# Kernel optimization log

Hardware: AMD Instinct MI355X
Metric: run time of the kernel (lower is better)

Reference implementation:

```python
import jax, jax.numpy as jnp
import numpy as np

EPS = 1e-12

def _l2norm(v, axis):
    n = jnp.sqrt(jnp.sum(v * v, axis=axis, keepdims=True))
    return v / jnp.maximum(n, EPS)

def setup_inputs() -> dict:
    key = jax.random.key(0)
    k1, k2, k3, k4 = jax.random.split(key, 4)
    N, T, D, K = 8, 2048, 512, 64
    x = jax.random.normal(k1, (N, T, D), dtype=jnp.float32)
    W = jax.random.normal(k2, (K, D), dtype=jnp.float32) * (1.0 / np.sqrt(D))  # Conv1d(k=1) weight squeezed
    b = jax.random.normal(k3, (K,), dtype=jnp.float32) * 0.01
    centroids = jax.random.uniform(k4, (K, D), dtype=jnp.float32)
    return {"x": x, "W": W, "b": b, "centroids": centroids}

def reference(x, W, b, centroids):
    N, T, D = x.shape
    K = centroids.shape[0]
    # L2-normalize descriptors along feature dim
    xn = _l2norm(x, axis=2)                                  # [N,T,D]
    # Conv1d with kernel_size=1 == per-timestep linear: [N,K,T] logits over clusters
    logits = jnp.einsum('ntd,kd->nkt', xn, W) + b[None, :, None]
    a = jax.nn.softmax(logits, axis=1)                       # soft assignment over K
    # Algebraically equal to sum_t a[n,k,t] * (xn[n,t,:] - c[k,:])
    vlad = jnp.einsum('nkt,ntd->nkd', a, xn) \
         - jnp.sum(a, axis=2)[:, :, None] * centroids[None]  # [N,K,D]
    vlad = _l2norm(vlad, axis=2)                             # intra-normalize per cluster
    vlad = vlad.reshape(N, K * D)
    return _l2norm(vlad, axis=1)                             # global L2 normalize
```

## Files before the change

### kernel.cpp

```cpp
#include <hip/hip_runtime.h>
#include <math.h>

#define EPS 1e-12f
#define NN 8
#define TT 2048
#define DD 512
#define KK 64

typedef short short8 __attribute__((ext_vector_type(8)));
typedef float floatx4 __attribute__((ext_vector_type(4)));

__device__ __forceinline__ unsigned short f2bf(float f) {
    unsigned int u = __float_as_uint(f);
    u += 0x7FFFu + ((u >> 16) & 1u);
    return (unsigned short)(u >> 16);
}
__device__ __forceinline__ unsigned int pack2(float a, float b) {
    return (unsigned int)f2bf(a) | ((unsigned int)f2bf(b) << 16);
}


__global__ __launch_bounds__(256) void kA(const float* __restrict__ x,
                                          const float* __restrict__ W,
                                          const float* __restrict__ bias,
                                          unsigned short* __restrict__ xb,
                                          unsigned short* __restrict__ aTs,
                                          float* __restrict__ asumP) {
    __shared__ unsigned short sW[32768];
    __shared__ float sRed[256];

    const int tid = threadIdx.x;

    const int w = tid >> 6, lane = tid & 63;
    const int l = lane & 15, q = lane >> 4;
    const int row0 = blockIdx.x * 64 + w * 16;
    const int row = row0 + l;
    const int n = row0 >> 11;
    const int tl0 = row0 & (TT - 1);

    const float* xr = x + (size_t)row * DD;
    unsigned short* xo = xb + (size_t)row * DD;
    short8 fragA[16];
    float ssq = 0.0f;
#pragma unroll
    for (int s = 0; s < 16; ++s) {
        float4 u0 = *(const float4*)(xr + s * 32 + q * 8);
        float4 u1 = *(const float4*)(xr + s * 32 + q * 8 + 4);
        ssq += u0.x*u0.x + u0.y*u0.y + u0.z*u0.z + u0.w*u0.w
             + u1.x*u1.x + u1.y*u1.y + u1.z*u1.z + u1.w*u1.w;
        uint4 pk;
        pk.x = pack2(u0.x, u0.y); pk.y = pack2(u0.z, u0.w);
        pk.z = pack2(u1.x, u1.y); pk.w = pack2(u1.z, u1.w);
        union { uint4 u; short8 s8; } cvt; cvt.u = pk;
        fragA[s] = cvt.s8;
        *(uint4*)(xo + s * 32 + q * 8) = pk;
    }

    {
        const int sp = tid >> 4, hp = (tid >> 2) & 3, qp = tid & 3;
        const float* wsrc = W + (size_t)(hp * 16) * DD + sp * 32 + qp * 8;
        unsigned short* wdst = sW + (size_t)tid * 128;
#pragma unroll
        for (int j = 0; j < 16; ++j) {
            float4 u0 = *(const float4*)(wsrc + (size_t)j * DD);
            float4 u1 = *(const float4*)(wsrc + (size_t)j * DD + 4);
            uint4 pk;
            pk.x = pack2(u0.x, u0.y); pk.y = pack2(u0.z, u0.w);
            pk.z = pack2(u1.x, u1.y); pk.w = pack2(u1.z, u1.w);
            *(uint4*)(wdst + j * 8) = pk;
        }
    }

    ssq += __shfl_xor(ssq, 16, 64);
    ssq += __shfl_xor(ssq, 32, 64);
    float st = 1.0f / fmaxf(sqrtf(ssq), EPS);

    __syncthreads();

    floatx4 acc[4];
#pragma unroll
    for (int h = 0; h < 4; ++h) acc[h] = floatx4{0.f, 0.f, 0.f, 0.f};
#pragma unroll
    for (int s = 0; s < 16; ++s) {
#pragma unroll
        for (int h = 0; h < 4; ++h) {
            short8 wf = *(const short8*)(sW + ((size_t)((s * 4 + h) * 64) + lane) * 8);
            acc[h] = __builtin_amdgcn_mfma_f32_16x16x32_bf16(fragA[s], wf, acc[h], 0, 0, 0);
        }
    }

    float sr[4];
#pragma unroll
    for (int r = 0; r < 4; ++r) sr[r] = __shfl(st, 4 * q + r, 64);
    float bj[4];
#pragma unroll
    for (int h = 0; h < 4; ++h) bj[h] = bias[h * 16 + l];

    float av[4][4];
#pragma unroll
    for (int r = 0; r < 4; ++r) {
        float v0 = acc[0][r] * sr[r] + bj[0], v1 = acc[1][r] * sr[r] + bj[1];
        float v2 = acc[2][r] * sr[r] + bj[2], v3 = acc[3][r] * sr[r] + bj[3];
        float m = fmaxf(fmaxf(v0, v1), fmaxf(v2, v3));
#pragma unroll
        for (int msk = 1; msk <= 8; msk <<= 1) m = fmaxf(m, __shfl_xor(m, msk, 64));
        float e0 = __expf(v0 - m), e1 = __expf(v1 - m), e2 = __expf(v2 - m), e3 = __expf(v3 - m);
        float ss = e0 + e1 + e2 + e3;
#pragma unroll
        for (int msk = 1; msk <= 8; msk <<= 1) ss += __shfl_xor(ss, msk, 64);
        float inv = 1.0f / ss;
        av[0][r] = e0 * inv; av[1][r] = e1 * inv; av[2][r] = e2 * inv; av[3][r] = e3 * inv;
    }

#pragma unroll
    for (int h = 0; h < 4; ++h) {
        uint2 p;
        p.x = pack2(av[h][0] * sr[0], av[h][1] * sr[1]);
        p.y = pack2(av[h][2] * sr[2], av[h][3] * sr[3]);
        *(uint2*)(aTs + ((size_t)(n * KK + h * 16 + l)) * TT + tl0 + 4 * q) = p;
    }

#pragma unroll
    for (int h = 0; h < 4; ++h) {
        float sh = av[h][0] + av[h][1] + av[h][2] + av[h][3];
        sh += __shfl_xor(sh, 16, 64);
        sh += __shfl_xor(sh, 32, 64);
        if (q == 0) sRed[w * 64 + h * 16 + l] = sh;
    }
    __syncthreads();
    if (tid < 64) {
        float s0 = sRed[tid] + sRed[64 + tid] + sRed[128 + tid] + sRed[192 + tid];
        asumP[(size_t)blockIdx.x * 64 + tid] = s0;
    }
}

__global__ __launch_bounds__(256) void kB(const unsigned short* __restrict__ xb,
                                          const unsigned short* __restrict__ aTs,
                                          float* __restrict__ part) {
    __shared__ unsigned char smem[17408];
    unsigned short* sX0 = (unsigned short*)smem;
    unsigned short* sX1 = sX0 + 4096;
    float* sT = (float*)smem;

    const int tid = threadIdx.x;
    const int wv = tid >> 6, lane = tid & 63;
    const int l = lane & 15, q = lane >> 4;
    const int bid = blockIdx.x;
    const int low = bid & 63;
    const int n = low >> 3, tc = low & 7, dt = bid >> 6;

    const int ts = tid & 63, dq = tid >> 6;
    const unsigned short* xbase = xb + ((size_t)(n * TT + tc * 256)) * DD + dt * 64 + dq * 16;
    const int g = ts >> 3, t7 = ts & 7;

#define STAGE(S, BUF)                                                          \
    {                                                                          \
        const unsigned short* p_ = xbase + (size_t)((S) * 64 + ts) * DD;       \
        unsigned short vals[16];                                               \
        *(uint4*)(vals) = *(const uint4*)(p_);                                 \
        *(uint4*)(vals + 8) = *(const uint4*)(p_ + 8);                         \
        _Pragma("unroll")                                                      \
        for (int e = 0; e < 16; ++e) {                                         \
            int d_ = dq * 16 + e;                                              \
            (BUF)[d_ * 64 + ((g ^ (d_ & 7)) << 3) + t7] = vals[e];             \
        }                                                                      \
    }

    floatx4 acc[4];
#pragma unroll
    for (int nt = 0; nt < 4; ++nt) acc[nt] = floatx4{0.f, 0.f, 0.f, 0.f};
    const unsigned short* abase = aTs + ((size_t)(n * KK + wv * 16 + l)) * TT + tc * 256;

    STAGE(0, sX0);
    __syncthreads();
#pragma unroll
    for (int s = 0; s < 4; ++s) {
        unsigned short* cur = (s & 1) ? sX1 : sX0;
        unsigned short* nxt = (s & 1) ? sX0 : sX1;
        if (s < 3) {
            if (s == 0) STAGE(1, nxt)
            else if (s == 1) STAGE(2, nxt)
            else STAGE(3, nxt)
        }
#pragma unroll
        for (int kb = 0; kb < 2; ++kb) {
            short8 af = *(const short8*)(abase + s * 64 + kb * 32 + q * 8);
            int gg = q + 4 * kb;
#pragma unroll
            for (int nt = 0; nt < 4; ++nt) {
                int d = nt * 16 + l;
                short8 bf = *(const short8*)(cur + d * 64 + ((gg ^ (d & 7)) << 3));
                acc[nt] = __builtin_amdgcn_mfma_f32_16x16x32_bf16(af, bf, acc[nt], 0, 0, 0);
            }
        }
        __syncthreads();
    }
#undef STAGE

#pragma unroll
    for (int nt = 0; nt < 4; ++nt)
#pragma unroll
        for (int r = 0; r < 4; ++r)
            sT[(wv * 16 + 4 * q + r) * 68 + nt * 16 + l] = acc[nt][r];
    __syncthreads();

    float* pbase = part + ((size_t)(tc * 512 + n * KK)) * DD + dt * 64;
    const int fq = tid & 15, kr = tid >> 4;
#pragma unroll
    for (int i = 0; i < 4; ++i) {
        int k = i * 16 + kr;
        float4 val = *(float4*)(sT + k * 68 + fq * 4);
        *(float4*)(pbase + (size_t)k * DD + fq * 4) = val;
    }
}

__global__ __launch_bounds__(128) void kC(const float* __restrict__ part,
                                          const float* __restrict__ asumP,
                                          const float* __restrict__ cent,
                                          float* __restrict__ out) {
    __shared__ float red[2];
    __shared__ float sAsum;
    const int nk = blockIdx.x;
    const int n = nk >> 6, k = nk & 63;
    const int tid = threadIdx.x;

    if (tid < 32) {
        float p = asumP[(size_t)(n * 32 + tid) * 64 + k];
#pragma unroll
        for (int m = 16; m >= 1; m >>= 1) p += __shfl_xor(p, m, 64);
        if (tid == 0) sAsum = p;
    }
    __syncthreads();
    float as = sAsum;

    float4 cc = ((const float4*)(cent + (size_t)k * DD))[tid];
    float4 a4 = make_float4(-as * cc.x, -as * cc.y, -as * cc.z, -as * cc.w);
#pragma unroll
    for (int tc = 0; tc < 8; ++tc) {
        float4 p = ((const float4*)(part + ((size_t)(tc * 512 + nk)) * DD))[tid];
        a4.x += p.x; a4.y += p.y; a4.z += p.z; a4.w += p.w;
    }
    float ssq = a4.x*a4.x + a4.y*a4.y + a4.z*a4.z + a4.w*a4.w;
#pragma unroll
    for (int m = 32; m >= 1; m >>= 1) ssq += __shfl_xor(ssq, m, 64);
    if ((tid & 63) == 0) red[tid >> 6] = ssq;
    __syncthreads();
    float nr = sqrtf(red[0] + red[1]);
    float sc = 1.0f / (fmaxf(nr, EPS) * 8.0f);
    a4.x *= sc; a4.y *= sc; a4.z *= sc; a4.w *= sc;
    ((float4*)(out + (size_t)nk * DD))[tid] = a4;
}

extern "C" void kernel_launch(void* const* d_in, const int* in_sizes, int n_in,
                              void* d_out, int out_size, void* d_ws, size_t ws_size,
                              hipStream_t stream) {
    const float* x    = (const float*)d_in[0];
    const float* W    = (const float*)d_in[1];
    const float* b    = (const float*)d_in[2];
    const float* cent = (const float*)d_in[3];
    float* out = (float*)d_out;

    float* w = (float*)d_ws;
    unsigned short* xb  = (unsigned short*)(w + 0);
    unsigned short* aTs = (unsigned short*)(w + 4194304);
    float* part  = w + 4718592;
    float* asumP = w + 6815744;

    hipLaunchKernelGGL(kA, dim3(256), dim3(256), 0, stream, x, W, b, xb, aTs, asumP);
    hipLaunchKernelGGL(kB, dim3(512), dim3(256), 0, stream, xb, aTs, part);
    hipLaunchKernelGGL(kC, dim3(512), dim3(128), 0, stream, part, asumP, cent, out);
}
```

Measured before the change: 96.47 us.

## Fuse three kernels into one cooperative kernel with grid-wide syncs

New measurement: 162.7 us. 68.7% more time.

```diff
diff --git a/kernel.cpp b/kernel.cpp
--- a/kernel.cpp
+++ b/kernel.cpp
@@ -1,5 +1,8 @@
 #include <hip/hip_runtime.h>
+#include <hip/hip_cooperative_groups.h>
 #include <math.h>
+
+namespace cg = cooperative_groups;
 
 #define EPS 1e-12f
 #define NN 8
@@ -20,235 +23,250 @@
 }
 
 
-__global__ __launch_bounds__(256) void kA(const float* __restrict__ x,
-                                          const float* __restrict__ W,
-                                          const float* __restrict__ bias,
-                                          unsigned short* __restrict__ xb,
-                                          unsigned short* __restrict__ aTs,
-                                          float* __restrict__ asumP) {
-    __shared__ unsigned short sW[32768];
-    __shared__ float sRed[256];
+__global__ __launch_bounds__(256) void mega(const float* __restrict__ x,
+                                            const float* __restrict__ W,
+                                            const float* __restrict__ bias,
+                                            const float* __restrict__ cent,
+                                            unsigned short* __restrict__ xb,
+                                            unsigned short* __restrict__ aTs,
+                                            float* __restrict__ part,
+                                            float* __restrict__ asumP,
+                                            float* __restrict__ out) {
+    __shared__ __align__(16) unsigned char smem[66560];
+    cg::grid_group gg_ = cg::this_grid();
 
     const int tid = threadIdx.x;
-
+    const int bid = blockIdx.x;
     const int w = tid >> 6, lane = tid & 63;
     const int l = lane & 15, q = lane >> 4;
-    const int row0 = blockIdx.x * 64 + w * 16;
-    const int row = row0 + l;
-    const int n = row0 >> 11;
-    const int tl0 = row0 & (TT - 1);
-
-    const float* xr = x + (size_t)row * DD;
-    unsigned short* xo = xb + (size_t)row * DD;
-    short8 fragA[16];
-    float ssq = 0.0f;
-#pragma unroll
-    for (int s = 0; s < 16; ++s) {
-        float4 u0 = *(const float4*)(xr + s * 32 + q * 8);
-        float4 u1 = *(const float4*)(xr + s * 32 + q * 8 + 4);
-        ssq += u0.x*u0.x + u0.y*u0.y + u0.z*u0.z + u0.w*u0.w
-             + u1.x*u1.x + u1.y*u1.y + u1.z*u1.z + u1.w*u1.w;
-        uint4 pk;
-        pk.x = pack2(u0.x, u0.y); pk.y = pack2(u0.z, u0.w);
-        pk.z = pack2(u1.x, u1.y); pk.w = pack2(u1.z, u1.w);
-        union { uint4 u; short8 s8; } cvt; cvt.u = pk;
-        fragA[s] = cvt.s8;
-        *(uint4*)(xo + s * 32 + q * 8) = pk;
-    }
 
     {
-        const int sp = tid >> 4, hp = (tid >> 2) & 3, qp = tid & 3;
-        const float* wsrc = W + (size_t)(hp * 16) * DD + sp * 32 + qp * 8;
-        unsigned short* wdst = sW + (size_t)tid * 128;
-#pragma unroll
-        for (int j = 0; j < 16; ++j) {
-            float4 u0 = *(const float4*)(wsrc + (size_t)j * DD);
-            float4 u1 = *(const float4*)(wsrc + (size_t)j * DD + 4);
+        unsigned short* sW = (unsigned short*)smem;
+        float* sRed = (float*)(smem + 65536);
+
+        const int row0 = bid * 64 + w * 16;
+        const int row = row0 + l;
+        const int n = row0 >> 11;
+        const int tl0 = row0 & (TT - 1);
+
+        const float* xr = x + (size_t)row * DD;
+        unsigned short* xo = xb + (size_t)row * DD;
+        short8 fragA[16];
+        float ssq = 0.0f;
+#pragma unroll
+        for (int s = 0; s < 16; ++s) {
+            float4 u0 = *(const float4*)(xr + s * 32 + q * 8);
+            float4 u1 = *(const float4*)(xr + s * 32 + q * 8 + 4);
+            ssq += u0.x*u0.x + u0.y*u0.y + u0.z*u0.z + u0.w*u0.w
+                 + u1.x*u1.x + u1.y*u1.y + u1.z*u1.z + u1.w*u1.w;
             uint4 pk;
             pk.x = pack2(u0.x, u0.y); pk.y = pack2(u0.z, u0.w);
             pk.z = pack2(u1.x, u1.y); pk.w = pack2(u1.z, u1.w);
-            *(uint4*)(wdst + j * 8) = pk;
-        }
-    }
-
-    ssq += __shfl_xor(ssq, 16, 64);
-    ssq += __shfl_xor(ssq, 32, 64);
-    float st = 1.0f / fmaxf(sqrtf(ssq), EPS);
-
-    __syncthreads();
-
-    floatx4 acc[4];
-#pragma unroll
-    for (int h = 0; h < 4; ++h) acc[h] = floatx4{0.f, 0.f, 0.f, 0.f};
-#pragma unroll
-    for (int s = 0; s < 16; ++s) {
+            union { uint4 u; short8 s8; } cvt; cvt.u = pk;
+            fragA[s] = cvt.s8;
+            *(uint4*)(xo + s * 32 + q * 8) = pk;
+        }
+
+        {
+            const int sp = tid >> 4, hp = (tid >> 2) & 3, qp = tid & 3;
+            const float* wsrc = W + (size_t)(hp * 16) * DD + sp * 32 + qp * 8;
+            unsigned short* wdst = sW + (size_t)tid * 128;
+#pragma unroll
+            for (int j = 0; j < 16; ++j) {
+                float4 u0 = *(const float4*)(wsrc + (size_t)j * DD);
+                float4 u1 = *(const float4*)(wsrc + (size_t)j * DD + 4);
+                uint4 pk;
+                pk.x = pack2(u0.x, u0.y); pk.y = pack2(u0.z, u0.w);
+                pk.z = pack2(u1.x, u1.y); pk.w = pack2(u1.z, u1.w);
+                *(uint4*)(wdst + j * 8) = pk;
+            }
+        }
+
+        ssq += __shfl_xor(ssq, 16, 64);
+        ssq += __shfl_xor(ssq, 32, 64);
+        float st = 1.0f / fmaxf(sqrtf(ssq), EPS);
+
+        __syncthreads();
+
+        floatx4 acc[4];
+#pragma unroll
+        for (int h = 0; h < 4; ++h) acc[h] = floatx4{0.f, 0.f, 0.f, 0.f};
+#pragma unroll
+        for (int s = 0; s < 16; ++s) {
+#pragma unroll
+            for (int h = 0; h < 4; ++h) {
+                short8 wf = *(const short8*)(sW + ((size_t)((s * 4 + h) * 64) + lane) * 8);
+                acc[h] = __builtin_amdgcn_mfma_f32_16x16x32_bf16(fragA[s], wf, acc[h], 0, 0, 0);
+            }
+        }
+
+        float sr[4];
+#pragma unroll
+        for (int r = 0; r < 4; ++r) sr[r] = __shfl(st, 4 * q + r, 64);
+        float bj[4];
+#pragma unroll
+        for (int h = 0; h < 4; ++h) bj[h] = bias[h * 16 + l];
+
+        float av[4][4];
+#pragma unroll
+        for (int r = 0; r < 4; ++r) {
+            float v0 = acc[0][r] * sr[r] + bj[0], v1 = acc[1][r] * sr[r] + bj[1];
+            float v2 = acc[2][r] * sr[r] + bj[2], v3 = acc[3][r] * sr[r] + bj[3];
+            float m = fmaxf(fmaxf(v0, v1), fmaxf(v2, v3));
+#pragma unroll
+            for (int msk = 1; msk <= 8; msk <<= 1) m = fmaxf(m, __shfl_xor(m, msk, 64));
+            float e0 = __expf(v0 - m), e1 = __expf(v1 - m), e2 = __expf(v2 - m), e3 = __expf(v3 - m);
+            float ss = e0 + e1 + e2 + e3;
+#pragma unroll
+            for (int msk = 1; msk <= 8; msk <<= 1) ss += __shfl_xor(ss, msk, 64);
+            float inv = 1.0f / ss;
+            av[0][r] = e0 * inv; av[1][r] = e1 * inv; av[2][r] = e2 * inv; av[3][r] = e3 * inv;
+        }
+
 #pragma unroll
         for (int h = 0; h < 4; ++h) {
-            short8 wf = *(const short8*)(sW + ((size_t)((s * 4 + h) * 64) + lane) * 8);
-            acc[h] = __builtin_amdgcn_mfma_f32_16x16x32_bf16(fragA[s], wf, acc[h], 0, 0, 0);
-        }
-    }
-
-    float sr[4];
-#pragma unroll
-    for (int r = 0; r < 4; ++r) sr[r] = __shfl(st, 4 * q + r, 64);
-    float bj[4];
-#pragma unroll
-    for (int h = 0; h < 4; ++h) bj[h] = bias[h * 16 + l];
-
-    float av[4][4];
-#pragma unroll
-    for (int r = 0; r < 4; ++r) {
-        float v0 = acc[0][r] * sr[r] + bj[0], v1 = acc[1][r] * sr[r] + bj[1];
-        float v2 = acc[2][r] * sr[r] + bj[2], v3 = acc[3][r] * sr[r] + bj[3];
-        float m = fmaxf(fmaxf(v0, v1), fmaxf(v2, v3));
-#pragma unroll
-        for (int msk = 1; msk <= 8; msk <<= 1) m = fmaxf(m, __shfl_xor(m, msk, 64));
-        float e0 = __expf(v0 - m), e1 = __expf(v1 - m), e2 = __expf(v2 - m), e3 = __expf(v3 - m);
-        float ss = e0 + e1 + e2 + e3;
-#pragma unroll
-        for (int msk = 1; msk <= 8; msk <<= 1) ss += __shfl_xor(ss, msk, 64);
-        float inv = 1.0f / ss;
-        av[0][r] = e0 * inv; av[1][r] = e1 * inv; av[2][r] = e2 * inv; av[3][r] = e3 * inv;
-    }
-
-#pragma unroll
-    for (int h = 0; h < 4; ++h) {
-        uint2 p;
-        p.x = pack2(av[h][0] * sr[0], av[h][1] * sr[1]);
-        p.y = pack2(av[h][2] * sr[2], av[h][3] * sr[3]);
-        *(uint2*)(aTs + ((size_t)(n * KK + h * 16 + l)) * TT + tl0 + 4 * q) = p;
-    }
-
-#pragma unroll
-    for (int h = 0; h < 4; ++h) {
-        float sh = av[h][0] + av[h][1] + av[h][2] + av[h][3];
-        sh += __shfl_xor(sh, 16, 64);
-        sh += __shfl_xor(sh, 32, 64);
-        if (q == 0) sRed[w * 64 + h * 16 + l] = sh;
-    }
-    __syncthreads();
-    if (tid < 64) {
-        float s0 = sRed[tid] + sRed[64 + tid] + sRed[128 + tid] + sRed[192 + tid];
-        asumP[(size_t)blockIdx.x * 64 + tid] = s0;
-    }
-}
-
-__global__ __launch_bounds__(256) void kB(const unsigned short* __restrict__ xb,
-                                          const unsigned short* __restrict__ aTs,
-                                          float* __restrict__ part) {
-    __shared__ unsigned char smem[17408];
-    unsigned short* sX0 = (unsigned short*)smem;
-    unsigned short* sX1 = sX0 + 4096;
-    float* sT = (float*)smem;
-
-    const int tid = threadIdx.x;
-    const int wv = tid >> 6, lane = tid & 63;
-    const int l = lane & 15, q = lane >> 4;
-    const int bid = blockIdx.x;
-    const int low = bid & 63;
-    const int n = low >> 3, tc = low & 7, dt = bid >> 6;
-
-    const int ts = tid & 63, dq = tid >> 6;
-    const unsigned short* xbase = xb + ((size_t)(n * TT + tc * 256)) * DD + dt * 64 + dq * 16;
-    const int g = ts >> 3, t7 = ts & 7;
+            uint2 p;
+            p.x = pack2(av[h][0] * sr[0], av[h][1] * sr[1]);
+            p.y = pack2(av[h][2] * sr[2], av[h][3] * sr[3]);
+            *(uint2*)(aTs + ((size_t)(n * KK + h * 16 + l)) * TT + tl0 + 4 * q) = p;
+        }
+
+#pragma unroll
+        for (int h = 0; h < 4; ++h) {
+            float sh = av[h][0] + av[h][1] + av[h][2] + av[h][3];
+            sh += __shfl_xor(sh, 16, 64);
+            sh += __shfl_xor(sh, 32, 64);
+            if (q == 0) sRed[w * 64 + h * 16 + l] = sh;
+        }
+        __syncthreads();
+        if (tid < 64) {
+            float s0 = sRed[tid] + sRed[64 + tid] + sRed[128 + tid] + sRed[192 + tid];
+            asumP[(size_t)bid * 64 + tid] = s0;
+        }
+    }
+
+    gg_.sync();
+
+    {
+        unsigned short* sX0 = (unsigned short*)smem;
+        unsigned short* sX1 = sX0 + 8192;
+        float* sT = (float*)smem;
+
+        const int low = bid & 63;
+        const int n = low >> 3, tc = low & 7, dt0 = bid >> 6;
+
+        const int ts = tid & 63, dq = tid >> 6;
+        const unsigned short* xbase = xb + ((size_t)(n * TT + tc * 256)) * DD + dt0 * 64 + dq * 16;
+        const int g = ts >> 3, t7 = ts & 7;
 
 #define STAGE(S, BUF)                                                          \
     {                                                                          \
         const unsigned short* p_ = xbase + (size_t)((S) * 64 + ts) * DD;       \
-        unsigned short vals[16];                                               \
-        *(uint4*)(vals) = *(const uint4*)(p_);                                 \
-        *(uint4*)(vals + 8) = *(const uint4*)(p_ + 8);                         \
+        unsigned short vals[32];                                               \
+        *(uint4*)(vals)      = *(const uint4*)(p_);                            \
+        *(uint4*)(vals + 8)  = *(const uint4*)(p_ + 8);                        \
+        *(uint4*)(vals + 16) = *(const uint4*)(p_ + 256);                      \
+        *(uint4*)(vals + 24) = *(const uint4*)(p_ + 256 + 8);                  \
         _Pragma("unroll")                                                      \
         for (int e = 0; e < 16; ++e) {                                         \
             int d_ = dq * 16 + e;                                              \
             (BUF)[d_ * 64 + ((g ^ (d_ & 7)) << 3) + t7] = vals[e];             \
         }                                                                      \
-    }
-
-    floatx4 acc[4];
-#pragma unroll
-    for (int nt = 0; nt < 4; ++nt) acc[nt] = floatx4{0.f, 0.f, 0.f, 0.f};
-    const unsigned short* abase = aTs + ((size_t)(n * KK + wv * 16 + l)) * TT + tc * 256;
-
-    STAGE(0, sX0);
-    __syncthreads();
-#pragma unroll
-    for (int s = 0; s < 4; ++s) {
-        unsigned short* cur = (s & 1) ? sX1 : sX0;
-        unsigned short* nxt = (s & 1) ? sX0 : sX1;
-        if (s < 3) {
-            if (s == 0) STAGE(1, nxt)
-            else if (s == 1) STAGE(2, nxt)
-            else STAGE(3, nxt)
-        }
-#pragma unroll
-        for (int kb = 0; kb < 2; ++kb) {
-            short8 af = *(const short8*)(abase + s * 64 + kb * 32 + q * 8);
-            int gg = q + 4 * kb;
-#pragma unroll
-            for (int nt = 0; nt < 4; ++nt) {
-                int d = nt * 16 + l;
-                short8 bf = *(const short8*)(cur + d * 64 + ((gg ^ (d & 7)) << 3));
-                acc[nt] = __builtin_amdgcn_mfma_f32_16x16x32_bf16(af, bf, acc[nt], 0, 0, 0);
-            }
-        }
-        __syncthreads();
-    }
+        _Pragma("unroll")                                                      \
+        for (int e = 0; e < 16; ++e) {                                         \
+            int d_ = 64 + dq * 16 + e;                                         \
+            (BUF)[d_ * 64 + ((g ^ (d_ & 7)) << 3) + t7] = vals[16 + e];        \
+        }                                                                      \
+    }
+
+        floatx4 acc[8];
+#pragma unroll
+        for (int nt = 0; nt < 8; ++nt) acc[nt] = floatx4{0.f, 0.f, 0.f, 0.f};
+        const unsigned short* abase = aTs + ((size_t)(n * KK + w * 16 + l)) * TT + tc * 256;
+
+        STAGE(0, sX0);
+        __syncthreads();
+#pragma unroll
+        for (int s = 0; s < 4; ++s) {
+            unsigned short* cur = (s & 1) ? sX1 : sX0;
+            unsigned short* nxt = (s & 1) ? sX0 : sX1;
+            if (s < 3) {
+                if (s == 0) STAGE(1, nxt)
+                else if (s == 1) STAGE(2, nxt)
+                else STAGE(3, nxt)
+            }
+#pragma unroll
+            for (int kb = 0; kb < 2; ++kb) {
+                short8 af = *(const short8*)(abase + s * 64 + kb * 32 + q * 8);
+                int ggi = q + 4 * kb;
+#pragma unroll
+                for (int nt = 0; nt < 8; ++nt) {
+                    int d = nt * 16 + l;
+                    short8 bf = *(const short8*)(cur + d * 64 + ((ggi ^ (d & 7)) << 3));
+                    acc[nt] = __builtin_amdgcn_mfma_f32_16x16x32_bf16(af, bf, acc[nt], 0, 0, 0);
+                }
+            }
+            __syncthreads();
+        }
 #undef STAGE
 
 #pragma unroll
-    for (int nt = 0; nt < 4; ++nt)
-#pragma unroll
-        for (int r = 0; r < 4; ++r)
-            sT[(wv * 16 + 4 * q + r) * 68 + nt * 16 + l] = acc[nt][r];
-    __syncthreads();
-
-    float* pbase = part + ((size_t)(tc * 512 + n * KK)) * DD + dt * 64;
-    const int fq = tid & 15, kr = tid >> 4;
-#pragma unroll
-    for (int i = 0; i < 4; ++i) {
-        int k = i * 16 + kr;
-        float4 val = *(float4*)(sT + k * 68 + fq * 4);
-        *(float4*)(pbase + (size_t)k * DD + fq * 4) = val;
-    }
-}
-
-__global__ __launch_bounds__(128) void kC(const float* __restrict__ part,
-                                          const float* __restrict__ asumP,
-                                          const float* __restrict__ cent,
-                                          float* __restrict__ out) {
-    __shared__ float red[2];
-    __shared__ float sAsum;
-    const int nk = blockIdx.x;
-    const int n = nk >> 6, k = nk & 63;
-    const int tid = threadIdx.x;
-
-    if (tid < 32) {
-        float p = asumP[(size_t)(n * 32 + tid) * 64 + k];
-#pragma unroll
-        for (int m = 16; m >= 1; m >>= 1) p += __shfl_xor(p, m, 64);
-        if (tid == 0) sAsum = p;
-    }
-    __syncthreads();
-    float as = sAsum;
-
-    float4 cc = ((const float4*)(cent + (size_t)k * DD))[tid];
-    float4 a4 = make_float4(-as * cc.x, -as * cc.y, -as * cc.z, -as * cc.w);
-#pragma unroll
-    for (int tc = 0; tc < 8; ++tc) {
-        float4 p = ((const float4*)(part + ((size_t)(tc * 512 + nk)) * DD))[tid];
-        a4.x += p.x; a4.y += p.y; a4.z += p.z; a4.w += p.w;
-    }
-    float ssq = a4.x*a4.x + a4.y*a4.y + a4.z*a4.z + a4.w*a4.w;
-#pragma unroll
-    for (int m = 32; m >= 1; m >>= 1) ssq += __shfl_xor(ssq, m, 64);
-    if ((tid & 63) == 0) red[tid >> 6] = ssq;
-    __syncthreads();
-    float nr = sqrtf(red[0] + red[1]);
-    float sc = 1.0f / (fmaxf(nr, EPS) * 8.0f);
-    a4.x *= sc; a4.y *= sc; a4.z *= sc; a4.w *= sc;
-    ((float4*)(out + (size_t)nk * DD))[tid] = a4;
+        for (int nt = 0; nt < 8; ++nt)
+#pragma unroll
+            for (int r = 0; r < 4; ++r)
+                sT[(w * 16 + 4 * q + r) * 132 + nt * 16 + l] = acc[nt][r];
+        __syncthreads();
+
+        float* pbase = part + ((size_t)(tc * 512 + n * KK)) * DD + dt0 * 64;
+        const int fq = tid & 31, kr = tid >> 5;
+#pragma unroll
+        for (int i = 0; i < 8; ++i) {
+            int k = i * 8 + kr;
+            int dl = fq * 4;
+            int off = dl + ((dl >> 6) * 192);
+            float4 val = *(float4*)(sT + k * 132 + dl);
+            *(float4*)(pbase + (size_t)k * DD + off) = val;
+        }
+        __syncthreads();
+    }
+
+    gg_.sync();
+
+    {
+        float* sAsum = (float*)smem;
+        float* sRedC = (float*)smem + 8;
+
+        const int half = tid >> 7, lt = tid & 127;
+        const int nk = bid * 2 + half;
+        const int n = nk >> 6, k = nk & 63;
+
+        if (lt < 32) {
+            float p = asumP[(size_t)(n * 32 + lt) * 64 + k];
+#pragma unroll
+            for (int m = 16; m >= 1; m >>= 1) p += __shfl_xor(p, m, 64);
+            if (lt == 0) sAsum[half] = p;
+        }
+        __syncthreads();
+        float as = sAsum[half];
+
+        float4 cc = ((const float4*)(cent + (size_t)k * DD))[lt];
+        float4 a4 = make_float4(-as * cc.x, -as * cc.y, -as * cc.z, -as * cc.w);
+#pragma unroll
+        for (int tc = 0; tc < 8; ++tc) {
+            float4 p = ((const float4*)(part + ((size_t)(tc * 512 + nk)) * DD))[lt];
+            a4.x += p.x; a4.y += p.y; a4.z += p.z; a4.w += p.w;
+        }
+        float ssq = a4.x*a4.x + a4.y*a4.y + a4.z*a4.z + a4.w*a4.w;
+#pragma unroll
+        for (int m = 32; m >= 1; m >>= 1) ssq += __shfl_xor(ssq, m, 64);
+        const int wave = tid >> 6;
+        if ((tid & 63) == 0) sRedC[wave] = ssq;
+        __syncthreads();
+        float nr = sqrtf(sRedC[2 * half] + sRedC[2 * half + 1]);
+        float sc = 1.0f / (fmaxf(nr, EPS) * 8.0f);
+        a4.x *= sc; a4.y *= sc; a4.z *= sc; a4.w *= sc;
+        ((float4*)(out + (size_t)nk * DD))[lt] = a4;
+    }
 }
 
 extern "C" void kernel_launch(void* const* d_in, const int* in_sizes, int n_in,
@@ -266,7 +284,9 @@
     float* part  = w + 4718592;
     float* asumP = w + 6815744;
 
-    hipLaunchKernelGGL(kA, dim3(256), dim3(256), 0, stream, x, W, b, xb, aTs, asumP);
-    hipLaunchKernelGGL(kB, dim3(512), dim3(256), 0, stream, xb, aTs, part);
-    hipLaunchKernelGGL(kC, dim3(512), dim3(128), 0, stream, part, asumP, cent, out);
-}
+    void* args[] = {(void*)&x, (void*)&W, (void*)&b, (void*)&cent,
+                    (void*)&xb, (void*)&aTs, (void*)&part, (void*)&asumP,
+                    (void*)&out};
+    hipLaunchCooperativeKernel((const void*)mega, dim3(256), dim3(256),
+                               args, 0, stream);
+}
```

## Store x transposed in bf16 and compute full-T VLAD per block with fused norms

Applied to the files above, without the earlier changes.

Result: slower. 111.7 us (+15.8%).

```diff
diff --git a/kernel.cpp b/kernel.cpp
--- a/kernel.cpp
+++ b/kernel.cpp
@@ -23,23 +23,26 @@
 __global__ __launch_bounds__(256) void kA(const float* __restrict__ x,
                                           const float* __restrict__ W,
                                           const float* __restrict__ bias,
-                                          unsigned short* __restrict__ xb,
+                                          unsigned short* __restrict__ xbT,
                                           unsigned short* __restrict__ aTs,
-                                          float* __restrict__ asumP) {
-    __shared__ unsigned short sW[32768];
-    __shared__ float sRed[256];
+                                          float* __restrict__ asumP,
+                                          float* __restrict__ norms) {
+    __shared__ __align__(16) unsigned char smem[67584];
+    unsigned short* sW = (unsigned short*)smem;
+    unsigned short* sT = (unsigned short*)smem;
+    float* sRed = (float*)(smem + 66560);
 
     const int tid = threadIdx.x;
-
+    const int bid = blockIdx.x;
     const int w = tid >> 6, lane = tid & 63;
     const int l = lane & 15, q = lane >> 4;
-    const int row0 = blockIdx.x * 64 + w * 16;
+    const int row0 = bid * 64 + w * 16;
     const int row = row0 + l;
     const int n = row0 >> 11;
     const int tl0 = row0 & (TT - 1);
+    const int tblk = (bid * 64) & (TT - 1);
 
     const float* xr = x + (size_t)row * DD;
-    unsigned short* xo = xb + (size_t)row * DD;
     short8 fragA[16];
     float ssq = 0.0f;
 #pragma unroll
@@ -53,7 +56,6 @@
         pk.z = pack2(u1.x, u1.y); pk.w = pack2(u1.z, u1.w);
         union { uint4 u; short8 s8; } cvt; cvt.u = pk;
         fragA[s] = cvt.s8;
-        *(uint4*)(xo + s * 32 + q * 8) = pk;
     }
 
     {
@@ -130,125 +132,102 @@
     __syncthreads();
     if (tid < 64) {
         float s0 = sRed[tid] + sRed[64 + tid] + sRed[128 + tid] + sRed[192 + tid];
-        asumP[(size_t)blockIdx.x * 64 + tid] = s0;
-    }
-}
-
-__global__ __launch_bounds__(256) void kB(const unsigned short* __restrict__ xb,
+        asumP[(size_t)bid * 64 + tid] = s0;
+    }
+
+#pragma unroll
+    for (int s = 0; s < 16; ++s)
+        *(short8*)(sT + (size_t)(w * 16 + l) * 520 + s * 32 + q * 8) = fragA[s];
+    __syncthreads();
+
+#pragma unroll
+    for (int c = 0; c < 2; ++c) {
+        int d = tid + c * 256;
+        const unsigned short* colb = sT + d;
+        unsigned short* ob = xbT + ((size_t)(n * DD + d)) * TT + tblk;
+#pragma unroll
+        for (int jj = 0; jj < 8; ++jj) {
+            uint4 pk;
+            pk.x = (unsigned int)colb[(jj * 8 + 0) * 520] | ((unsigned int)colb[(jj * 8 + 1) * 520] << 16);
+            pk.y = (unsigned int)colb[(jj * 8 + 2) * 520] | ((unsigned int)colb[(jj * 8 + 3) * 520] << 16);
+            pk.z = (unsigned int)colb[(jj * 8 + 4) * 520] | ((unsigned int)colb[(jj * 8 + 5) * 520] << 16);
+            pk.w = (unsigned int)colb[(jj * 8 + 6) * 520] | ((unsigned int)colb[(jj * 8 + 7) * 520] << 16);
+            *(uint4*)(ob + jj * 8) = pk;
+        }
+    }
+
+    if (bid == 0) { norms[tid] = 0.0f; norms[tid + 256] = 0.0f; }
+}
+
+__global__ __launch_bounds__(256) void kB(const unsigned short* __restrict__ xbT,
                                           const unsigned short* __restrict__ aTs,
-                                          float* __restrict__ part) {
-    __shared__ unsigned char smem[17408];
-    unsigned short* sX0 = (unsigned short*)smem;
-    unsigned short* sX1 = sX0 + 4096;
-    float* sT = (float*)smem;
-
+                                          const float* __restrict__ asumP,
+                                          const float* __restrict__ cent,
+                                          float* __restrict__ vpre,
+                                          float* __restrict__ norms) {
+    __shared__ float sAs[16];
     const int tid = threadIdx.x;
-    const int wv = tid >> 6, lane = tid & 63;
+    const int w = tid >> 6, lane = tid & 63;
     const int l = lane & 15, q = lane >> 4;
     const int bid = blockIdx.x;
-    const int low = bid & 63;
-    const int n = low >> 3, tc = low & 7, dt = bid >> 6;
-
-    const int ts = tid & 63, dq = tid >> 6;
-    const unsigned short* xbase = xb + ((size_t)(n * TT + tc * 256)) * DD + dt * 64 + dq * 16;
-    const int g = ts >> 3, t7 = ts & 7;
-
-#define STAGE(S, BUF)                                                          \
-    {                                                                          \
-        const unsigned short* p_ = xbase + (size_t)((S) * 64 + ts) * DD;       \
-        unsigned short vals[16];                                               \
-        *(uint4*)(vals) = *(const uint4*)(p_);                                 \
-        *(uint4*)(vals + 8) = *(const uint4*)(p_ + 8);                         \
-        _Pragma("unroll")                                                      \
-        for (int e = 0; e < 16; ++e) {                                         \
-            int d_ = dq * 16 + e;                                              \
-            (BUF)[d_ * 64 + ((g ^ (d_ & 7)) << 3) + t7] = vals[e];             \
-        }                                                                      \
-    }
-
-    floatx4 acc[4];
-#pragma unroll
-    for (int nt = 0; nt < 4; ++nt) acc[nt] = floatx4{0.f, 0.f, 0.f, 0.f};
-    const unsigned short* abase = aTs + ((size_t)(n * KK + wv * 16 + l)) * TT + tc * 256;
-
-    STAGE(0, sX0);
-    __syncthreads();
-#pragma unroll
-    for (int s = 0; s < 4; ++s) {
-        unsigned short* cur = (s & 1) ? sX1 : sX0;
-        unsigned short* nxt = (s & 1) ? sX0 : sX1;
-        if (s < 3) {
-            if (s == 0) STAGE(1, nxt)
-            else if (s == 1) STAGE(2, nxt)
-            else STAGE(3, nxt)
-        }
-#pragma unroll
-        for (int kb = 0; kb < 2; ++kb) {
-            short8 af = *(const short8*)(abase + s * 64 + kb * 32 + q * 8);
-            int gg = q + 4 * kb;
-#pragma unroll
-            for (int nt = 0; nt < 4; ++nt) {
-                int d = nt * 16 + l;
-                short8 bf = *(const short8*)(cur + d * 64 + ((gg ^ (d & 7)) << 3));
-                acc[nt] = __builtin_amdgcn_mfma_f32_16x16x32_bf16(af, bf, acc[nt], 0, 0, 0);
-            }
-        }
-        __syncthreads();
-    }
-#undef STAGE
-
-#pragma unroll
-    for (int nt = 0; nt < 4; ++nt)
-#pragma unroll
-        for (int r = 0; r < 4; ++r)
-            sT[(wv * 16 + 4 * q + r) * 68 + nt * 16 + l] = acc[nt][r];
-    __syncthreads();
-
-    float* pbase = part + ((size_t)(tc * 512 + n * KK)) * DD + dt * 64;
-    const int fq = tid & 15, kr = tid >> 4;
-#pragma unroll
-    for (int i = 0; i < 4; ++i) {
-        int k = i * 16 + kr;
-        float4 val = *(float4*)(sT + k * 68 + fq * 4);
-        *(float4*)(pbase + (size_t)k * DD + fq * 4) = val;
-    }
-}
-
-__global__ __launch_bounds__(128) void kC(const float* __restrict__ part,
-                                          const float* __restrict__ asumP,
-                                          const float* __restrict__ cent,
+    const int kq = bid >> 6, n = (bid >> 3) & 7, dq = bid & 7;
+    const int k0 = kq * 16;
+    const int dbase = dq * 64 + w * 16;
+
+    if (tid < 16) sAs[tid] = 0.0f;
+    __syncthreads();
+    {
+        const int kk = tid & 15, chunk = tid >> 4;
+        float p = asumP[(size_t)(n * 32 + chunk) * 64 + k0 + kk]
+                + asumP[(size_t)(n * 32 + 16 + chunk) * 64 + k0 + kk];
+        p += __shfl_xor(p, 16, 64);
+        p += __shfl_xor(p, 32, 64);
+        if (q == 0) atomicAdd(&sAs[kk], p);
+    }
+
+    const unsigned short* ap = aTs + ((size_t)(n * KK + k0 + l)) * TT + q * 8;
+    const unsigned short* bp = xbT + ((size_t)(n * DD + dbase + l)) * TT + q * 8;
+    floatx4 a0 = {0.f, 0.f, 0.f, 0.f}, a1 = a0, a2 = a0, a3 = a0;
+#pragma unroll
+    for (int s = 0; s < 64; s += 4) {
+        a0 = __builtin_amdgcn_mfma_f32_16x16x32_bf16(*(const short8*)(ap + (s + 0) * 32),
+                                                     *(const short8*)(bp + (s + 0) * 32), a0, 0, 0, 0);
+        a1 = __builtin_amdgcn_mfma_f32_16x16x32_bf16(*(const short8*)(ap + (s + 1) * 32),
+                                                     *(const short8*)(bp + (s + 1) * 32), a1, 0, 0, 0);
+        a2 = __builtin_amdgcn_mfma_f32_16x16x32_bf16(*(const short8*)(ap + (s + 2) * 32),
+                                                     *(const short8*)(bp + (s + 2) * 32), a2, 0, 0, 0);
+        a3 = __builtin_amdgcn_mfma_f32_16x16x32_bf16(*(const short8*)(ap + (s + 3) * 32),
+                                                     *(const short8*)(bp + (s + 3) * 32), a3, 0, 0, 0);
+    }
+    floatx4 acc;
+#pragma unroll
+    for (int r = 0; r < 4; ++r) acc[r] = (a0[r] + a1[r]) + (a2[r] + a3[r]);
+
+    __syncthreads();
+
+    const int d = dbase + l;
+#pragma unroll
+    for (int r = 0; r < 4; ++r) {
+        int k = k0 + 4 * q + r;
+        float val = acc[r] - sAs[4 * q + r] * cent[(size_t)k * DD + d];
+        vpre[((size_t)(n * KK + k)) * DD + d] = val;
+        float s2 = val * val;
+#pragma unroll
+        for (int msk = 1; msk <= 8; msk <<= 1) s2 += __shfl_xor(s2, msk, 64);
+        if (l == 0) atomicAdd(&norms[n * KK + k], s2);
+    }
+}
+
+__global__ __launch_bounds__(128) void kC(const float* __restrict__ vpre,
+                                          const float* __restrict__ norms,
                                           float* __restrict__ out) {
-    __shared__ float red[2];
-    __shared__ float sAsum;
     const int nk = blockIdx.x;
-    const int n = nk >> 6, k = nk & 63;
     const int tid = threadIdx.x;
-
-    if (tid < 32) {
-        float p = asumP[(size_t)(n * 32 + tid) * 64 + k];
-#pragma unroll
-        for (int m = 16; m >= 1; m >>= 1) p += __shfl_xor(p, m, 64);
-        if (tid == 0) sAsum = p;
-    }
-    __syncthreads();
-    float as = sAsum;
-
-    float4 cc = ((const float4*)(cent + (size_t)k * DD))[tid];
-    float4 a4 = make_float4(-as * cc.x, -as * cc.y, -as * cc.z, -as * cc.w);
-#pragma unroll
-    for (int tc = 0; tc < 8; ++tc) {
-        float4 p = ((const float4*)(part + ((size_t)(tc * 512 + nk)) * DD))[tid];
-        a4.x += p.x; a4.y += p.y; a4.z += p.z; a4.w += p.w;
-    }
-    float ssq = a4.x*a4.x + a4.y*a4.y + a4.z*a4.z + a4.w*a4.w;
-#pragma unroll
-    for (int m = 32; m >= 1; m >>= 1) ssq += __shfl_xor(ssq, m, 64);
-    if ((tid & 63) == 0) red[tid >> 6] = ssq;
-    __syncthreads();
-    float nr = sqrtf(red[0] + red[1]);
+    float nr = sqrtf(norms[nk]);
     float sc = 1.0f / (fmaxf(nr, EPS) * 8.0f);
-    a4.x *= sc; a4.y *= sc; a4.z *= sc; a4.w *= sc;
-    ((float4*)(out + (size_t)nk * DD))[tid] = a4;
+    float4 v4 = ((const float4*)(vpre + (size_t)nk * DD))[tid];
+    v4.x *= sc; v4.y *= sc; v4.z *= sc; v4.w *= sc;
+    ((float4*)(out + (size_t)nk * DD))[tid] = v4;
 }
 
 extern "C" void kernel_launch(void* const* d_in, const int* in_sizes, int n_in,
@@ -261,12 +240,13 @@
     float* out = (float*)d_out;
 
     float* w = (float*)d_ws;
-    unsigned short* xb  = (unsigned short*)(w + 0);
+    unsigned short* xbT = (unsigned short*)(w + 0);
     unsigned short* aTs = (unsigned short*)(w + 4194304);
-    float* part  = w + 4718592;
-    float* asumP = w + 6815744;
-
-    hipLaunchKernelGGL(kA, dim3(256), dim3(256), 0, stream, x, W, b, xb, aTs, asumP);
-    hipLaunchKernelGGL(kB, dim3(512), dim3(256), 0, stream, xb, aTs, part);
-    hipLaunchKernelGGL(kC, dim3(512), dim3(128), 0, stream, part, asumP, cent, out);
-}
+    float* vpre  = w + 4718592;
+    float* asumP = w + 4980736;
+    float* norms = w + 4997120;
+
+    hipLaunchKernelGGL(kA, dim3(256), dim3(256), 0, stream, x, W, b, xbT, aTs, asumP, norms);
+    hipLaunchKernelGGL(kB, dim3(256), dim3(256), 0, stream, xbT, aTs, asumP, cent, vpre, norms);
+    hipLaunchKernelGGL(kC, dim3(512), dim3(128), 0, stream, vpre, norms, out);
+}
```
